# Kernel tuning notes

Measured on AMD Instinct MI355X. Metric: run time of the kernel, lower is better.

The kernel has to match this reference:

```python
import jax, jax.numpy as jnp
import numpy as np

IN, OUT, RANK = 4096, 4096, 8
ALPHA = 8.0

def _quantize_int8(x):
    # row-wise symmetric int8 quantization (matches torch _quantize_int8)
    scale = jnp.max(jnp.abs(x), axis=1) / 127.0              # [rows]
    q = jnp.round(x / jnp.clip(scale, 1e-12)[:, None]).astype(jnp.int8)
    return q, scale


def setup_inputs() -> dict:
    key = jax.random.key(0)
    k_x, k_w, k_a, k_b = jax.random.split(key, 4)
    x = jax.random.normal(k_x, (8192, IN), dtype=jnp.float32)
    # simulate quantizing a pretrained fp32 weight [OUT, IN]
    w = jax.random.normal(k_w, (OUT, IN), dtype=jnp.float32) * 0.02
    w_scale = jnp.max(jnp.abs(w), axis=1) / 127.0
    weight_i8 = jnp.round(w / jnp.clip(w_scale, 1e-12)[:, None]).astype(jnp.int8)
    weight_scale = w_scale.astype(jnp.float32)               # [OUT]
    # LoRA params (lora_b random instead of zeros so output is nontrivial)
    lora_a = jax.random.normal(k_a, (RANK, IN), dtype=jnp.float32) * (1.0 / np.sqrt(IN))
    lora_b = jax.random.normal(k_b, (OUT, RANK), dtype=jnp.float32) * 0.02
    return {"x": x, "weight_i8": weight_i8, "weight_scale": weight_scale,
            "lora_a": lora_a, "lora_b": lora_b}


def reference(x, weight_i8, weight_scale, lora_a, lora_b):
    # quantize_act=True path: int8 activation quant + int8 GEMM (int32 accum) + dequant
    x_i8, x_scale = _quantize_int8(x)                         # [T, IN] int8, [T]
    out_i32 = jnp.matmul(x_i8, weight_i8.T, preferred_element_type=jnp.int32)  # [T, OUT]
    out = out_i32.astype(jnp.float32) * x_scale[:, None] * weight_scale[None, :]
    # LoRA low-rank add: x @ A^T @ B^T * (alpha / rank)
    out = out + (x @ lora_a.T) @ lora_b.T * (ALPHA / RANK)
    return out
```

## Files before the change

### kernel.cpp

```cpp
#include <hip/hip_runtime.h>
#include <stdint.h>

#define T_DIM   8192
#define IN_DIM  4096
#define OUT_DIM 4096
#define RANK    8

typedef int v4i __attribute__((ext_vector_type(4)));

__device__ __forceinline__ void async_copy16(const void* g, void* l) {
  __builtin_amdgcn_global_load_lds(
      (const __attribute__((address_space(1))) void*)g,
      (__attribute__((address_space(3))) void*)l, 16, 0, 0);
}

__global__ __launch_bounds__(256) void pack_w(
    const int* __restrict__ w32, int8_t* __restrict__ w8)
{
  const int idx = blockIdx.x * 256 + threadIdx.x;
  const int4 v = ((const int4*)w32)[idx];
  char4 q;
  q.x = (signed char)v.x; q.y = (signed char)v.y;
  q.z = (signed char)v.z; q.w = (signed char)v.w;
  ((char4*)w8)[idx] = q;
}

#define QROWS 4
__global__ __launch_bounds__(256) void quant_x(
    const float* __restrict__ x, const float* __restrict__ lora_a,
    int8_t* __restrict__ x_i8, float* __restrict__ x_scale,
    float* __restrict__ xa)
{
  const int tid = threadIdx.x;
  const int wave = tid >> 6;
  const size_t row0 = (size_t)blockIdx.x * QROWS;
  __shared__ float redm[4][QROWS];
  __shared__ float redd[4][QROWS][RANK];

  const float4* xr = (const float4*)(x + row0 * IN_DIM);
  float4 xv[QROWS][4];
#pragma unroll
  for (int r = 0; r < QROWS; ++r)
#pragma unroll
    for (int c = 0; c < 4; ++c)
      xv[r][c] = xr[r * 1024 + c * 256 + tid];

  float am[QROWS];
#pragma unroll
  for (int r = 0; r < QROWS; ++r) {
    float m = 0.f;
#pragma unroll
    for (int c = 0; c < 4; ++c)
      m = fmaxf(m, fmaxf(fmaxf(fabsf(xv[r][c].x), fabsf(xv[r][c].y)),
                         fmaxf(fabsf(xv[r][c].z), fabsf(xv[r][c].w))));
    am[r] = m;
  }
#pragma unroll
  for (int off = 32; off > 0; off >>= 1)
#pragma unroll
    for (int r = 0; r < QROWS; ++r)
      am[r] = fmaxf(am[r], __shfl_xor(am[r], off, 64));
  if ((tid & 63) == 0)
#pragma unroll
    for (int r = 0; r < QROWS; ++r) redm[wave][r] = am[r];

  float dot[QROWS][RANK];
#pragma unroll
  for (int rk = 0; rk < RANK; ++rk) {
    const float4* ar = (const float4*)(lora_a + (size_t)rk * IN_DIM);
    float4 av[4];
#pragma unroll
    for (int c = 0; c < 4; ++c) av[c] = ar[c * 256 + tid];
#pragma unroll
    for (int r = 0; r < QROWS; ++r) {
      float s = 0.f;
#pragma unroll
      for (int c = 0; c < 4; ++c)
        s += xv[r][c].x * av[c].x + xv[r][c].y * av[c].y +
             xv[r][c].z * av[c].z + xv[r][c].w * av[c].w;
      dot[r][rk] = s;
    }
  }
#pragma unroll
  for (int off = 32; off > 0; off >>= 1)
#pragma unroll
    for (int r = 0; r < QROWS; ++r)
#pragma unroll
      for (int rk = 0; rk < RANK; ++rk)
        dot[r][rk] += __shfl_xor(dot[r][rk], off, 64);
  if ((tid & 63) == 0)
#pragma unroll
    for (int r = 0; r < QROWS; ++r)
#pragma unroll
      for (int rk = 0; rk < RANK; ++rk) redd[wave][r][rk] = dot[r][rk];
  __syncthreads();

#pragma unroll
  for (int r = 0; r < QROWS; ++r) {
    const float amax = fmaxf(fmaxf(redm[0][r], redm[1][r]),
                             fmaxf(redm[2][r], redm[3][r]));
    const float scale = amax * (1.0f / 127.0f);
    const float inv = 1.0f / fmaxf(scale, 1e-12f);
    char4* qout = (char4*)(x_i8 + (row0 + r) * IN_DIM);
#pragma unroll
    for (int c = 0; c < 4; ++c) {
      char4 q;
      q.x = (signed char)(int)rintf(xv[r][c].x * inv);
      q.y = (signed char)(int)rintf(xv[r][c].y * inv);
      q.z = (signed char)(int)rintf(xv[r][c].z * inv);
      q.w = (signed char)(int)rintf(xv[r][c].w * inv);
      qout[c * 256 + tid] = q;
    }
    if (tid == 0) x_scale[row0 + r] = scale;
  }
  if (tid < QROWS * RANK) {
    const int r = tid >> 3, rk = tid & 7;
    xa[(row0 + r) * RANK + rk] =
        redd[0][r][rk] + redd[1][r][rk] + redd[2][r][rk] + redd[3][r][rk];
  }
}

__device__ __forceinline__ void stage_tile(const int8_t* aSrc, const int8_t* bSrc,
                                           int8_t* Lbuf, int ldsOff) {
  async_copy16(aSrc,                          Lbuf + ldsOff);
  async_copy16(aSrc + (size_t)128 * IN_DIM,   Lbuf + 8192 + ldsOff);
  async_copy16(bSrc,                          Lbuf + 16384 + ldsOff);
  async_copy16(bSrc + (size_t)128 * IN_DIM,   Lbuf + 24576 + ldsOff);
}

__device__ __forceinline__ void read_frags(const int8_t* base, int aOff, int bOff,
                                           v4i (&fa)[8], v4i (&fb)[4]) {
#pragma unroll
  for (int i = 0; i < 8; ++i) fa[i] = *(const v4i*)(base + aOff + i * 1024);
#pragma unroll
  for (int j = 0; j < 4; ++j) fb[j] = *(const v4i*)(base + 16384 + bOff + j * 1024);
}

__device__ __forceinline__ void mfma_cluster(const v4i (&fa)[8], const v4i (&fb)[4],
                                             v4i (&acc)[8][4]) {
  __builtin_amdgcn_s_setprio(1);
#pragma unroll
  for (int i = 0; i < 8; ++i)
#pragma unroll
    for (int j = 0; j < 4; ++j)
      acc[i][j] = __builtin_amdgcn_mfma_i32_16x16x64_i8(fa[i], fb[j], acc[i][j], 0, 0, 0);
  __builtin_amdgcn_s_setprio(0);
}

#define KSYNC() do {                                                   \
    asm volatile("s_waitcnt vmcnt(4) lgkmcnt(0)" ::: "memory");        \
    __builtin_amdgcn_sched_barrier(0);                                 \
    __builtin_amdgcn_s_barrier();                                      \
    __builtin_amdgcn_sched_barrier(0);                                 \
  } while (0)

__global__ __launch_bounds__(512) void gemm256_i8(
    const int8_t* __restrict__ A,
    const int8_t* __restrict__ B,
    const float* __restrict__ x_scale,
    const float* __restrict__ w_scale,
    const float* __restrict__ xa,
    const float* __restrict__ lora_b,
    float* __restrict__ out)
{
  __shared__ __align__(16) int8_t smem[3 * 32768];
  const int tid = threadIdx.x;

  const int orig = blockIdx.x;
  const int wgid = ((orig & 7) << 6) | (orig >> 3);
  const int by = wgid >> 4;
  const int bx = wgid & 15;
  const size_t arow0 = (size_t)by * 256;
  const size_t brow0 = (size_t)bx * 256;

  const int r_l = tid >> 2;
  const int qsw = ((tid & 3) ^ ((r_l >> 1) & 3)) << 4;
  const int8_t* aSrc = A + (arow0 + r_l) * IN_DIM + qsw;
  const int8_t* bSrc = B + (brow0 + r_l) * IN_DIM + qsw;
  const int ldsOff = tid << 4;

  const int lane = tid & 63;
  const int wave = tid >> 6;
  const int wr = wave >> 2, wc = wave & 3;
  const int m16 = lane & 15, quad = lane >> 4;
  const int sw = (quad ^ ((m16 >> 1) & 3)) << 4;
  const int aOff = (wr * 128 + m16) * 64 + sw;
  const int bOff = (wc * 64 + m16) * 64 + sw;

  v4i acc[8][4];
  const v4i vz = {0, 0, 0, 0};
#pragma unroll
  for (int i = 0; i < 8; ++i)
#pragma unroll
    for (int j = 0; j < 4; ++j) acc[i][j] = vz;

  v4i fa0[8], fb0[4], fa1[8], fb1[4];

  stage_tile(aSrc,       bSrc,       (int8_t*)smem,          ldsOff);
  stage_tile(aSrc + 64,  bSrc + 64,  (int8_t*)smem + 32768,  ldsOff);
  stage_tile(aSrc + 128, bSrc + 128, (int8_t*)smem + 65536,  ldsOff);
  asm volatile("s_waitcnt vmcnt(8)" ::: "memory");
  __builtin_amdgcn_sched_barrier(0);
  __builtin_amdgcn_s_barrier();
  __builtin_amdgcn_sched_barrier(0);
  read_frags((const int8_t*)smem, aOff, bOff, fa0, fb0);

  int sb = 0;
  int rb = 32768;
#pragma unroll 1
  for (int t = 0; t < 64; t += 2) {
    KSYNC();
    {
      const int ks = (t + 3 < 64 ? t + 3 : 63) * 64;
      stage_tile(aSrc + ks, bSrc + ks, (int8_t*)smem + sb, ldsOff);
      read_frags((const int8_t*)smem + rb, aOff, bOff, fa1, fb1);
      mfma_cluster(fa0, fb0, acc);
    }
    sb += 32768; if (sb == 98304) sb = 0;
    rb += 32768; if (rb == 98304) rb = 0;
    KSYNC();
    {
      const int ks = (t + 4 < 64 ? t + 4 : 63) * 64;
      stage_tile(aSrc + ks, bSrc + ks, (int8_t*)smem + sb, ldsOff);
      read_frags((const int8_t*)smem + rb, aOff, bOff, fa0, fb0);
      mfma_cluster(fa1, fb1, acc);
    }
    sb += 32768; if (sb == 98304) sb = 0;
    rb += 32768; if (rb == 98304) rb = 0;
  }

  asm volatile("s_waitcnt vmcnt(0) lgkmcnt(0)" ::: "memory");
  __syncthreads();
  float* fs   = (float*)smem;
  float* xs_s = fs;
  float* ws_s = fs + 256;
  float* xa_s = fs + 512;
  float* lb_s = fs + 2560;
  if (tid < 256) xs_s[tid] = x_scale[arow0 + tid];
  else           ws_s[tid - 256] = w_scale[brow0 + (tid - 256)];
  ((float4*)xa_s)[tid] = ((const float4*)(xa + arow0 * RANK))[tid];
  ((float4*)lb_s)[tid] = ((const float4*)(lora_b + brow0 * RANK))[tid];
  __syncthreads();

  float wscv[4];
  float4 lb0[4], lb1[4];
  int cols[4];
#pragma unroll
  for (int j = 0; j < 4; ++j) {
    const int c = wc * 64 + j * 16 + m16;
    cols[j] = c;
    wscv[j] = ws_s[c];
    lb0[j] = *(const float4*)(lb_s + c * RANK);
    lb1[j] = *(const float4*)(lb_s + c * RANK + 4);
  }
#pragma unroll
  for (int i = 0; i < 8; ++i) {
#pragma unroll
    for (int reg = 0; reg < 4; ++reg) {
      const int r = wr * 128 + i * 16 + quad * 4 + reg;
      const float xsc = xs_s[r];
      const float4 xa0 = *(const float4*)(xa_s + r * RANK);
      const float4 xa1 = *(const float4*)(xa_s + r * RANK + 4);
      float* orow = out + (arow0 + (size_t)r) * OUT_DIM + brow0;
#pragma unroll
      for (int j = 0; j < 4; ++j) {
        float v = (float)acc[i][j][reg] * xsc * wscv[j];
        v += xa0.x * lb0[j].x + xa0.y * lb0[j].y + xa0.z * lb0[j].z + xa0.w * lb0[j].w +
             xa1.x * lb1[j].x + xa1.y * lb1[j].y + xa1.z * lb1[j].z + xa1.w * lb1[j].w;
        orow[cols[j]] = v;
      }
    }
  }
}

extern "C" void kernel_launch(void* const* d_in, const int* in_sizes, int n_in,
                              void* d_out, int out_size, void* d_ws, size_t ws_size,
                              hipStream_t stream) {
  const float* x       = (const float*)d_in[0];
  const int*   w_i32   = (const int*)d_in[1];
  const float* w_scale = (const float*)d_in[2];
  const float* lora_a  = (const float*)d_in[3];
  const float* lora_b  = (const float*)d_in[4];
  float* out = (float*)d_out;

  int8_t* x_i8    = (int8_t*)d_ws;
  int8_t* w8      = x_i8 + (size_t)T_DIM * IN_DIM;
  float*  x_scale = (float*)(w8 + (size_t)OUT_DIM * IN_DIM);
  float*  xa      = x_scale + T_DIM;

  pack_w<<<(OUT_DIM * IN_DIM / 4) / 256, 256, 0, stream>>>(w_i32, w8);
  quant_x<<<T_DIM / QROWS, 256, 0, stream>>>(x, lora_a, x_i8, x_scale, xa);
  gemm256_i8<<<(T_DIM / 256) * (OUT_DIM / 256), 512, 0, stream>>>(
      x_i8, w8, x_scale, w_scale, xa, lora_b, out);
}
```

Baseline: 414.8 us.

## Switch int8 GEMM to 32x32x32 MFMA with triple-buffered static LDS schedule

Replaces the 16x16x64 int8 MFMA tiles with 32x32x32 MFMA, giving 4x2 v16i accumulators per wave. Fragments are now read from LDS just before each MFMA group instead of being double-buffered in registers. The K loop is restructured into a 3-stage rotation with fixed buffer offsets and an explicit epilogue, and launch bounds now request two blocks per CU. The intent is fewer LDS fragment reads per FLOP, less register pressure and simpler loop control, at the cost of less overlap between LDS reads and MFMA work. The epilogue row/column mapping is updated to match the 32x32 output layout.

```diff
diff --git a/kernel.cpp b/kernel.cpp
--- a/kernel.cpp
+++ b/kernel.cpp
@@ -6,7 +6,8 @@
 #define OUT_DIM 4096
 #define RANK    8
 
-typedef int v4i __attribute__((ext_vector_type(4)));
+typedef int v4i  __attribute__((ext_vector_type(4)));
+typedef int v16i __attribute__((ext_vector_type(16)));
 
 __device__ __forceinline__ void async_copy16(const void* g, void* l) {
   __builtin_amdgcn_global_load_lds(
@@ -120,6 +121,12 @@
   }
 }
 
+#define SYNC(n) do {                                      \
+    asm volatile("s_waitcnt vmcnt(" #n ")" ::: "memory"); \
+    __builtin_amdgcn_s_barrier();                         \
+    __builtin_amdgcn_sched_barrier(0);                    \
+  } while (0)
+
 __device__ __forceinline__ void stage_tile(const int8_t* aSrc, const int8_t* bSrc,
                                            int8_t* Lbuf, int ldsOff) {
   async_copy16(aSrc,                          Lbuf + ldsOff);
@@ -128,33 +135,27 @@
   async_copy16(bSrc + (size_t)128 * IN_DIM,   Lbuf + 24576 + ldsOff);
 }
 
-__device__ __forceinline__ void read_frags(const int8_t* base, int aOff, int bOff,
-                                           v4i (&fa)[8], v4i (&fb)[4]) {
-#pragma unroll
-  for (int i = 0; i < 8; ++i) fa[i] = *(const v4i*)(base + aOff + i * 1024);
-#pragma unroll
-  for (int j = 0; j < 4; ++j) fb[j] = *(const v4i*)(base + 16384 + bOff + j * 1024);
-}
-
-__device__ __forceinline__ void mfma_cluster(const v4i (&fa)[8], const v4i (&fb)[4],
-                                             v4i (&acc)[8][4]) {
-  __builtin_amdgcn_s_setprio(1);
-#pragma unroll
-  for (int i = 0; i < 8; ++i)
-#pragma unroll
-    for (int j = 0; j < 4; ++j)
-      acc[i][j] = __builtin_amdgcn_mfma_i32_16x16x64_i8(fa[i], fb[j], acc[i][j], 0, 0, 0);
-  __builtin_amdgcn_s_setprio(0);
-}
-
-#define KSYNC() do {                                                   \
-    asm volatile("s_waitcnt vmcnt(4) lgkmcnt(0)" ::: "memory");        \
-    __builtin_amdgcn_sched_barrier(0);                                 \
-    __builtin_amdgcn_s_barrier();                                      \
-    __builtin_amdgcn_sched_barrier(0);                                 \
-  } while (0)
-
-__global__ __launch_bounds__(512) void gemm256_i8(
+__device__ __forceinline__ void compute_tile(const int8_t* Lbuf, int aBase, int bBase,
+                                             int sw0, int sw1, v16i (&acc)[4][2]) {
+#pragma unroll
+  for (int ks = 0; ks < 2; ++ks) {
+    const int s = ks ? sw1 : sw0;
+    v4i aF[4], bF[2];
+#pragma unroll
+    for (int i = 0; i < 4; ++i) aF[i] = *(const v4i*)(Lbuf + aBase + i * 2048 + s);
+#pragma unroll
+    for (int j = 0; j < 2; ++j) bF[j] = *(const v4i*)(Lbuf + bBase + j * 2048 + s);
+    __builtin_amdgcn_s_setprio(1);
+#pragma unroll
+    for (int i = 0; i < 4; ++i)
+#pragma unroll
+      for (int j = 0; j < 2; ++j)
+        acc[i][j] = __builtin_amdgcn_mfma_i32_32x32x32_i8(aF[i], bF[j], acc[i][j], 0, 0, 0);
+    __builtin_amdgcn_s_setprio(0);
+  }
+}
+
+__global__ __launch_bounds__(512, 2) void gemm256_i8(
     const int8_t* __restrict__ A,
     const int8_t* __restrict__ B,
     const float* __restrict__ x_scale,
@@ -182,52 +183,48 @@
   const int lane = tid & 63;
   const int wave = tid >> 6;
   const int wr = wave >> 2, wc = wave & 3;
-  const int m16 = lane & 15, quad = lane >> 4;
-  const int sw = (quad ^ ((m16 >> 1) & 3)) << 4;
-  const int aOff = (wr * 128 + m16) * 64 + sw;
-  const int bOff = (wc * 64 + m16) * 64 + sw;
-
-  v4i acc[8][4];
-  const v4i vz = {0, 0, 0, 0};
-#pragma unroll
-  for (int i = 0; i < 8; ++i)
-#pragma unroll
-    for (int j = 0; j < 4; ++j) acc[i][j] = vz;
-
-  v4i fa0[8], fb0[4], fa1[8], fb1[4];
-
-  stage_tile(aSrc,       bSrc,       (int8_t*)smem,          ldsOff);
-  stage_tile(aSrc + 64,  bSrc + 64,  (int8_t*)smem + 32768,  ldsOff);
-  stage_tile(aSrc + 128, bSrc + 128, (int8_t*)smem + 65536,  ldsOff);
-  asm volatile("s_waitcnt vmcnt(8)" ::: "memory");
-  __builtin_amdgcn_sched_barrier(0);
+  const int r31 = lane & 31, khalf = lane >> 5;
+  const int rsw = (r31 >> 1) & 3;
+  const int sw0 = ((0 * 2 + khalf) ^ rsw) << 4;
+  const int sw1 = ((1 * 2 + khalf) ^ rsw) << 4;
+  const int aBase = (wr * 128 + r31) * 64;
+  const int bBase = 16384 + (wc * 64 + r31) * 64;
+
+  v16i acc[4][2];
+#pragma unroll
+  for (int i = 0; i < 4; ++i)
+#pragma unroll
+    for (int j = 0; j < 2; ++j)
+#pragma unroll
+      for (int e = 0; e < 16; ++e) acc[i][j][e] = 0;
+
+  stage_tile(aSrc,      bSrc,      (int8_t*)smem,         ldsOff);
+  stage_tile(aSrc + 64, bSrc + 64, (int8_t*)smem + 32768, ldsOff);
+
+#pragma unroll 1
+  for (int t = 0; t < 60; t += 3) {
+    SYNC(4);
+    stage_tile(aSrc + (t + 2) * 64, bSrc + (t + 2) * 64, (int8_t*)smem + 65536, ldsOff);
+    compute_tile((const int8_t*)smem, aBase, bBase, sw0, sw1, acc);
+    SYNC(4);
+    stage_tile(aSrc + (t + 3) * 64, bSrc + (t + 3) * 64, (int8_t*)smem, ldsOff);
+    compute_tile((const int8_t*)smem + 32768, aBase, bBase, sw0, sw1, acc);
+    SYNC(4);
+    stage_tile(aSrc + (t + 4) * 64, bSrc + (t + 4) * 64, (int8_t*)smem + 32768, ldsOff);
+    compute_tile((const int8_t*)smem + 65536, aBase, bBase, sw0, sw1, acc);
+  }
+  SYNC(4);
+  stage_tile(aSrc + 62 * 64, bSrc + 62 * 64, (int8_t*)smem + 65536, ldsOff);
+  compute_tile((const int8_t*)smem, aBase, bBase, sw0, sw1, acc);
+  SYNC(4);
+  stage_tile(aSrc + 63 * 64, bSrc + 63 * 64, (int8_t*)smem, ldsOff);
+  compute_tile((const int8_t*)smem + 32768, aBase, bBase, sw0, sw1, acc);
+  SYNC(4);
+  compute_tile((const int8_t*)smem + 65536, aBase, bBase, sw0, sw1, acc);
+  asm volatile("s_waitcnt vmcnt(0)" ::: "memory");
   __builtin_amdgcn_s_barrier();
   __builtin_amdgcn_sched_barrier(0);
-  read_frags((const int8_t*)smem, aOff, bOff, fa0, fb0);
-
-  int sb = 0;
-  int rb = 32768;
-#pragma unroll 1
-  for (int t = 0; t < 64; t += 2) {
-    KSYNC();
-    {
-      const int ks = (t + 3 < 64 ? t + 3 : 63) * 64;
-      stage_tile(aSrc + ks, bSrc + ks, (int8_t*)smem + sb, ldsOff);
-      read_frags((const int8_t*)smem + rb, aOff, bOff, fa1, fb1);
-      mfma_cluster(fa0, fb0, acc);
-    }
-    sb += 32768; if (sb == 98304) sb = 0;
-    rb += 32768; if (rb == 98304) rb = 0;
-    KSYNC();
-    {
-      const int ks = (t + 4 < 64 ? t + 4 : 63) * 64;
-      stage_tile(aSrc + ks, bSrc + ks, (int8_t*)smem + sb, ldsOff);
-      read_frags((const int8_t*)smem + rb, aOff, bOff, fa0, fb0);
-      mfma_cluster(fa1, fb1, acc);
-    }
-    sb += 32768; if (sb == 98304) sb = 0;
-    rb += 32768; if (rb == 98304) rb = 0;
-  }
+  compute_tile((const int8_t*)smem, aBase, bBase, sw0, sw1, acc);
 
   asm volatile("s_waitcnt vmcnt(0) lgkmcnt(0)" ::: "memory");
   __syncthreads();
@@ -242,28 +239,28 @@
   ((float4*)lb_s)[tid] = ((const float4*)(lora_b + brow0 * RANK))[tid];
   __syncthreads();
 
-  float wscv[4];
-  float4 lb0[4], lb1[4];
-  int cols[4];
-#pragma unroll
-  for (int j = 0; j < 4; ++j) {
-    const int c = wc * 64 + j * 16 + m16;
+  float wscv[2];
+  float4 lb0[2], lb1[2];
+  int cols[2];
+#pragma unroll
+  for (int j = 0; j < 2; ++j) {
+    const int c = wc * 64 + j * 32 + r31;
     cols[j] = c;
     wscv[j] = ws_s[c];
     lb0[j] = *(const float4*)(lb_s + c * RANK);
     lb1[j] = *(const float4*)(lb_s + c * RANK + 4);
   }
 #pragma unroll
-  for (int i = 0; i < 8; ++i) {
-#pragma unroll
-    for (int reg = 0; reg < 4; ++reg) {
-      const int r = wr * 128 + i * 16 + quad * 4 + reg;
+  for (int i = 0; i < 4; ++i) {
+#pragma unroll
+    for (int reg = 0; reg < 16; ++reg) {
+      const int r = wr * 128 + i * 32 + (reg & 3) + 8 * (reg >> 2) + 4 * khalf;
       const float xsc = xs_s[r];
       const float4 xa0 = *(const float4*)(xa_s + r * RANK);
       const float4 xa1 = *(const float4*)(xa_s + r * RANK + 4);
       float* orow = out + (arow0 + (size_t)r) * OUT_DIM + brow0;
 #pragma unroll
-      for (int j = 0; j < 4; ++j) {
+      for (int j = 0; j < 2; ++j) {
         float v = (float)acc[i][j][reg] * xsc * wscv[j];
         v += xa0.x * lb0[j].x + xa0.y * lb0[j].y + xa0.z * lb0[j].z + xa0.w * lb0[j].w +
              xa1.x * lb1[j].x + xa1.y * lb1[j].y + xa1.z * lb1[j].z + xa1.w * lb1[j].w;
```

Result: no change. 421.8 us (+1.7%).
